# Optimization experiments

Hardware: AMD Instinct MI355X
Metric: run time of the kernel (lower is better)

## Reference

```python
import jax, jax.numpy as jnp
import numpy as np

EMBED_DIM = 1024
NUM_HEADS = 16
HEAD_DIM = EMBED_DIM // NUM_HEADS


def setup_inputs() -> dict:
    key = jax.random.key(0)
    ks = jax.random.split(key, 5)
    x = jax.random.normal(ks[0], (2, 2048, EMBED_DIM), dtype=jnp.float32)
    s_in = 1.0 / np.sqrt(EMBED_DIM)
    W_qkv = jax.random.uniform(ks[1], (EMBED_DIM, 3 * EMBED_DIM), minval=-s_in, maxval=s_in, dtype=jnp.float32)
    b_qkv = jax.random.uniform(ks[2], (3 * EMBED_DIM,), minval=-s_in, maxval=s_in, dtype=jnp.float32)
    W_out = jax.random.uniform(ks[3], (EMBED_DIM, EMBED_DIM), minval=-s_in, maxval=s_in, dtype=jnp.float32)
    b_out = jax.random.uniform(ks[4], (EMBED_DIM,), minval=-s_in, maxval=s_in, dtype=jnp.float32)
    return {"x": x, "W_qkv": W_qkv, "b_qkv": b_qkv, "W_out": W_out, "b_out": b_out}


def reference(x, W_qkv, b_qkv, W_out, b_out):
    B, S, D = x.shape
    H, Dh = NUM_HEADS, HEAD_DIM
    qkv = x @ W_qkv + b_qkv                       # [B, S, 3D]
    q, k, v = jnp.split(qkv, 3, axis=-1)
    # [B, S, D] -> [B, H, S, Dh]
    q = q.reshape(B, S, H, Dh).transpose(0, 2, 1, 3)
    k = k.reshape(B, S, H, Dh).transpose(0, 2, 1, 3)
    v = v.reshape(B, S, H, Dh).transpose(0, 2, 1, 3)
    scores = jnp.einsum('bhqd,bhkd->bhqk', q, k) / jnp.sqrt(jnp.float32(Dh))
    probs = jax.nn.softmax(scores, axis=-1)       # [B, H, S, S]
    attn = jnp.einsum('bhqk,bhkd->bhqd', probs, v)
    attn = attn.transpose(0, 2, 1, 3).reshape(B, S, D)
    return attn @ W_out + b_out
```

## Files before the change

kernel.cpp:

```cpp
#include <hip/hip_runtime.h>
#include <hip/hip_bf16.h>

#define DEV __device__ __forceinline__

typedef __bf16 bf16x8 __attribute__((ext_vector_type(8)));
typedef float f32x4 __attribute__((ext_vector_type(4)));
typedef float f32x16 __attribute__((ext_vector_type(16)));
using u16 = unsigned short;
using u32 = unsigned int;

static constexpr int S = 2048;
static constexpr int D = 1024;
static constexpr float SCQ = 0.125f * 1.44269504088896340736f;

DEV u16 f2bf(float f) {
  unsigned u = __builtin_bit_cast(unsigned, f);
  u += 0x7fffu + ((u >> 16) & 1u);
  return (u16)(u >> 16);
}
DEV u16 f2bfr(float f) {
  return (u16)((__builtin_bit_cast(u32, f) + 0x8000u) >> 16);
}
DEV u32 pk2(float a, float b) {
  u32 ua = __builtin_bit_cast(u32, a) + 0x8000u;
  u32 ub = __builtin_bit_cast(u32, b) + 0x8000u;
  return __builtin_amdgcn_perm(ub, ua, 0x07060302);
}

__global__ __launch_bounds__(256) void k_prep(const float* __restrict__ x, u16* __restrict__ Xb,
                                              const float* __restrict__ Wqkv, u16* __restrict__ WqkvT,
                                              const float* __restrict__ Wout, u16* __restrict__ WoutT) {
  __shared__ float t[32][33];
  const int bid = blockIdx.x;
  const int tid = threadIdx.x;
  if (bid < 4096) {
    const int i = bid * 256 + tid;
    const float4 v = reinterpret_cast<const float4*>(x)[i];
    ushort4 o;
    o.x = f2bf(v.x); o.y = f2bf(v.y); o.z = f2bf(v.z); o.w = f2bf(v.w);
    reinterpret_cast<ushort4*>(Xb)[i] = o;
    return;
  }
  const float* in;
  u16* out;
  int R, C, bx, by;
  if (bid < 4096 + 3072) {
    const int b = bid - 4096;
    in = Wqkv; out = WqkvT; R = 1024; C = 3072;
    bx = b % 96; by = b / 96;
  } else {
    const int b = bid - 7168;
    in = Wout; out = WoutT; R = 1024; C = 1024;
    bx = b & 31; by = b >> 5;
  }
  const int tx = tid & 31, ty = tid >> 5;
  const int c0 = bx * 32, r0 = by * 32;
  for (int i = ty; i < 32; i += 8)
    t[i][tx] = in[(size_t)(r0 + i) * C + c0 + tx];
  __syncthreads();
  for (int i = ty; i < 32; i += 8)
    out[(size_t)(c0 + i) * R + r0 + tx] = f2bf(t[tx][i]);
}

template <int MODE, int TN>
__global__ __launch_bounds__(256) void k_gemm(const u16* __restrict__ A, const u16* __restrict__ Bt,
                                              const float* __restrict__ bias, int M, int N, int K,
                                              u16* __restrict__ Qb, u16* __restrict__ Kb,
                                              u16* __restrict__ Vt, float* __restrict__ outF) {
  constexpr int NJ = TN / 32;
  __shared__ u16 As[128][40];
  __shared__ u16 Bs[TN][40];
  const int tid = threadIdx.x;
  const int lane = tid & 63, wave = tid >> 6;
  const int l15 = lane & 15, quad = lane >> 4;
  const int m0 = blockIdx.y * 128, n0 = blockIdx.x * TN;
  const int wm = (wave >> 1) * 64, wn = (wave & 1) * (TN / 2);
  const int row0 = tid >> 2, c0 = (tid & 3) * 8;
  const int row1 = row0 + 64;

  f32x4 acc[4][NJ];
#pragma unroll
  for (int i = 0; i < 4; i++)
#pragma unroll
    for (int j = 0; j < NJ; j++) acc[i][j] = (f32x4){0.f, 0.f, 0.f, 0.f};

  uint4 pa0 = *reinterpret_cast<const uint4*>(&A[(size_t)(m0 + row0) * K + c0]);
  uint4 pa1 = *reinterpret_cast<const uint4*>(&A[(size_t)(m0 + row1) * K + c0]);
  uint4 pb0 = *reinterpret_cast<const uint4*>(&Bt[(size_t)(n0 + row0) * K + c0]);
  uint4 pb1;
  if constexpr (TN == 128) pb1 = *reinterpret_cast<const uint4*>(&Bt[(size_t)(n0 + row1) * K + c0]);

  for (int kk = 0; kk < K; kk += 32) {
    __syncthreads();
    *reinterpret_cast<uint4*>(&As[row0][c0]) = pa0;
    *reinterpret_cast<uint4*>(&As[row1][c0]) = pa1;
    *reinterpret_cast<uint4*>(&Bs[row0 & (TN - 1)][c0]) = pb0;
    if constexpr (TN == 128) *reinterpret_cast<uint4*>(&Bs[row1][c0]) = pb1;
    __syncthreads();
    if (kk + 32 < K) {
      pa0 = *reinterpret_cast<const uint4*>(&A[(size_t)(m0 + row0) * K + kk + 32 + c0]);
      pa1 = *reinterpret_cast<const uint4*>(&A[(size_t)(m0 + row1) * K + kk + 32 + c0]);
      pb0 = *reinterpret_cast<const uint4*>(&Bt[(size_t)(n0 + row0) * K + kk + 32 + c0]);
      if constexpr (TN == 128)
        pb1 = *reinterpret_cast<const uint4*>(&Bt[(size_t)(n0 + row1) * K + kk + 32 + c0]);
    }
    bf16x8 af[4], bfv[NJ];
#pragma unroll
    for (int i = 0; i < 4; i++)
      af[i] = *reinterpret_cast<const bf16x8*>(&As[wm + i * 16 + l15][quad * 8]);
#pragma unroll
    for (int j = 0; j < NJ; j++)
      bfv[j] = *reinterpret_cast<const bf16x8*>(&Bs[wn + j * 16 + l15][quad * 8]);
#pragma unroll
    for (int i = 0; i < 4; i++)
#pragma unroll
      for (int j = 0; j < NJ; j++)
        acc[i][j] = __builtin_amdgcn_mfma_f32_16x16x32_bf16(af[i], bfv[j], acc[i][j], 0, 0, 0);
  }

  if constexpr (MODE == 0) {
    __shared__ u16 LT[64][136];
    if (n0 >= 2048) {
      const int b = m0 >> 11, sbase = m0 & 2047;
#pragma unroll
      for (int p = 0; p < 2; p++) {
        __syncthreads();
        if ((wave & 1) == p) {
#pragma unroll
          for (int j = 0; j < NJ; j++) {
            const int n = n0 + wn + j * 16 + l15;
            const float vb = bias[n];
#pragma unroll
            for (int i = 0; i < 4; i++) {
              uint2 pw;
              pw.x = pk2(acc[i][j][0] + vb, acc[i][j][1] + vb);
              pw.y = pk2(acc[i][j][2] + vb, acc[i][j][3] + vb);
              *reinterpret_cast<uint2*>(&LT[j * 16 + l15][wm + i * 16 + quad * 4]) = pw;
            }
          }
        }
        __syncthreads();
        const int h = ((n0 - 2048) >> 6) + p;
        const int bh = b * 16 + h;
        const int nl = tid >> 2, cc = (tid & 3) * 32;
        u16* dst = &Vt[((size_t)bh * 64 + nl) * S + sbase + cc];
#pragma unroll
        for (int k = 0; k < 4; k++)
          reinterpret_cast<uint4*>(dst)[k] = *reinterpret_cast<const uint4*>(&LT[nl][cc + k * 8]);
      }
    } else {
#pragma unroll
      for (int i = 0; i < 4; i++) {
#pragma unroll
        for (int j = 0; j < NJ; j++) {
#pragma unroll
          for (int r = 0; r < 4; r++) {
            const int m = m0 + wm + i * 16 + quad * 4 + r;
            const int n = n0 + wn + j * 16 + l15;
            const float v = acc[i][j][r] + bias[n];
            const int h = (n >> 6) & 15, dh = n & 63;
            const int b = m >> 11, s = m & 2047;
            const int bh = b * 16 + h;
            if (n < 1024) Qb[((size_t)bh * S + s) * 64 + dh] = f2bfr(v * SCQ);
            else          Kb[((size_t)bh * S + s) * 64 + dh] = f2bfr(v);
          }
        }
      }
    }
  } else {
#pragma unroll
    for (int i = 0; i < 4; i++)
#pragma unroll
      for (int j = 0; j < NJ; j++)
#pragma unroll
        for (int r = 0; r < 4; r++) {
          const int m = m0 + wm + i * 16 + quad * 4 + r;
          const int n = n0 + wn + j * 16 + l15;
          outF[(size_t)m * N + n] = acc[i][j][r] + bias[n];
        }
  }
}

__global__ __launch_bounds__(256, 2) void k_attn(const u16* __restrict__ Qb,
                                                 const u16* __restrict__ Kb,
                                                 const u16* __restrict__ Vt,
                                                 u16* __restrict__ attnB) {
  __shared__ u16 Ks[64][72];
  __shared__ u16 Vs[64][72];
  __shared__ u16 Pl[4][32][72];
  const int bh = blockIdx.y;
  const int q0 = blockIdx.x * 128;
  const int tid = threadIdx.x;
  const int lane = tid & 63, wave = tid >> 6;
  const int l31 = lane & 31, hi = lane >> 5;
  const u16* Qh = Qb + (size_t)bh * S * 64;
  const u16* Kh = Kb + (size_t)bh * S * 64;
  const u16* Vh = Vt + (size_t)bh * 64 * S;
  const int qrow = q0 + wave * 32 + l31;
  bf16x8 qf[4];
#pragma unroll
  for (int f = 0; f < 4; f++)
    qf[f] = *reinterpret_cast<const bf16x8*>(&Qh[(size_t)qrow * 64 + f * 16 + hi * 8]);

  const int r0 = tid >> 3, c0 = (tid & 7) * 8;

  float li = 0.f;
  f32x16 o0, o1;
#pragma unroll
  for (int r = 0; r < 16; r++) { o0[r] = 0.f; o1[r] = 0.f; }

  uint4 pk0 = *reinterpret_cast<const uint4*>(&Kh[(size_t)r0 * 64 + c0]);
  uint4 pk1 = *reinterpret_cast<const uint4*>(&Kh[(size_t)(r0 + 32) * 64 + c0]);
  uint4 pv0 = *reinterpret_cast<const uint4*>(&Vh[(size_t)r0 * S + c0]);
  uint4 pv1 = *reinterpret_cast<const uint4*>(&Vh[(size_t)(r0 + 32) * S + c0]);

  for (int kb = 0; kb < S / 64; kb++) {
    __syncthreads();
    *reinterpret_cast<uint4*>(&Ks[r0][c0]) = pk0;
    *reinterpret_cast<uint4*>(&Ks[r0 + 32][c0]) = pk1;
    *reinterpret_cast<uint4*>(&Vs[r0][c0]) = pv0;
    *reinterpret_cast<uint4*>(&Vs[r0 + 32][c0]) = pv1;
    __syncthreads();
    if (kb + 1 < S / 64) {
      const u16* Kn = Kh + (size_t)(kb + 1) * 64 * 64;
      pk0 = *reinterpret_cast<const uint4*>(&Kn[(size_t)r0 * 64 + c0]);
      pk1 = *reinterpret_cast<const uint4*>(&Kn[(size_t)(r0 + 32) * 64 + c0]);
      pv0 = *reinterpret_cast<const uint4*>(&Vh[(size_t)r0 * S + (kb + 1) * 64 + c0]);
      pv1 = *reinterpret_cast<const uint4*>(&Vh[(size_t)(r0 + 32) * S + (kb + 1) * 64 + c0]);
    }
    f32x16 z[2];
#pragma unroll
    for (int kt = 0; kt < 2; kt++) {
#pragma unroll
      for (int r = 0; r < 16; r++) z[kt][r] = 0.f;
#pragma unroll
      for (int f = 0; f < 4; f++) {
        const bf16x8 a = *reinterpret_cast<const bf16x8*>(&Ks[kt * 32 + l31][f * 16 + hi * 8]);
        z[kt] = __builtin_amdgcn_mfma_f32_32x32x16_bf16(a, qf[f], z[kt], 0, 0, 0);
      }
    }
    float s0 = 0.f, s1 = 0.f, s2 = 0.f, s3 = 0.f;
#pragma unroll
    for (int kt = 0; kt < 2; kt++)
#pragma unroll
      for (int r = 0; r < 16; r++) {
        const float p = __builtin_amdgcn_exp2f(z[kt][r]);
        z[kt][r] = p;
        if ((r & 3) == 0) s0 += p; else if ((r & 3) == 1) s1 += p;
        else if ((r & 3) == 2) s2 += p; else s3 += p;
      }
    li += (s0 + s1) + (s2 + s3);
#pragma unroll
    for (int kt = 0; kt < 2; kt++)
#pragma unroll
      for (int g = 0; g < 4; g++) {
        uint2 pw;
        pw.x = pk2(z[kt][g * 4 + 0], z[kt][g * 4 + 1]);
        pw.y = pk2(z[kt][g * 4 + 2], z[kt][g * 4 + 3]);
        *reinterpret_cast<uint2*>(&Pl[wave][l31][kt * 32 + g * 8 + hi * 4]) = pw;
      }
#pragma unroll
    for (int f = 0; f < 4; f++) {
      const bf16x8 bp = *reinterpret_cast<const bf16x8*>(&Pl[wave][l31][f * 16 + hi * 8]);
      const bf16x8 av0 = *reinterpret_cast<const bf16x8*>(&Vs[l31][f * 16 + hi * 8]);
      const bf16x8 av1 = *reinterpret_cast<const bf16x8*>(&Vs[32 + l31][f * 16 + hi * 8]);
      o0 = __builtin_amdgcn_mfma_f32_32x32x16_bf16(av0, bp, o0, 0, 0, 0);
      o1 = __builtin_amdgcn_mfma_f32_32x32x16_bf16(av1, bp, o1, 0, 0, 0);
    }
  }
  li += __shfl_xor(li, 32);
  const float inv = 1.f / li;
#pragma unroll
  for (int dt = 0; dt < 2; dt++) {
    const f32x16& od = dt ? o1 : o0;
#pragma unroll
    for (int g = 0; g < 4; g++) {
      uint2 ow;
      ow.x = pk2(od[g * 4 + 0] * inv, od[g * 4 + 1] * inv);
      ow.y = pk2(od[g * 4 + 2] * inv, od[g * 4 + 3] * inv);
      *reinterpret_cast<uint2*>(&Pl[wave][l31][dt * 32 + g * 8 + hi * 4]) = ow;
    }
  }
  const int b = bh >> 4, h = bh & 15;
  const int mbase = b * S + q0 + wave * 32;
  const int qr = lane >> 1, ch = (lane & 1) * 32;
  u16* dst = &attnB[(size_t)(mbase + qr) * D + h * 64 + ch];
#pragma unroll
  for (int c = 0; c < 4; c++)
    reinterpret_cast<uint4*>(dst)[c] = *reinterpret_cast<const uint4*>(&Pl[wave][qr][ch + c * 8]);
}

extern "C" void kernel_launch(void* const* d_in, const int* in_sizes, int n_in,
                              void* d_out, int out_size, void* d_ws, size_t ws_size,
                              hipStream_t stream) {
  const float* x = (const float*)d_in[0];
  const float* Wqkv = (const float*)d_in[1];
  const float* bqkv = (const float*)d_in[2];
  const float* Wout = (const float*)d_in[3];
  const float* bout = (const float*)d_in[4];
  float* out = (float*)d_out;

  char* p = (char*)d_ws;
  u16* Xb = (u16*)p;    p += (size_t)4096 * 1024 * 2;
  u16* WqkvT = (u16*)p; p += (size_t)3072 * 1024 * 2;
  u16* WoutT = (u16*)p; p += (size_t)1024 * 1024 * 2;
  u16* Qb = (u16*)p;    p += (size_t)32 * 2048 * 64 * 2;
  u16* Kb = (u16*)p;    p += (size_t)32 * 2048 * 64 * 2;
  u16* Vt = (u16*)p;    p += (size_t)32 * 64 * 2048 * 2;
  u16* attnB = (u16*)p; p += (size_t)4096 * 1024 * 2;

  k_prep<<<4096 + 3072 + 1024, 256, 0, stream>>>(x, Xb, Wqkv, WqkvT, Wout, WoutT);
  k_gemm<0, 128><<<dim3(3072 / 128, 4096 / 128), 256, 0, stream>>>(
      Xb, WqkvT, bqkv, 4096, 3072, 1024, Qb, Kb, Vt, nullptr);
  k_attn<<<dim3(2048 / 128, 32), 256, 0, stream>>>(Qb, Kb, Vt, attnB);
  k_gemm<1, 64><<<dim3(1024 / 64, 4096 / 128), 256, 0, stream>>>(
      attnB, WoutT, bout, 4096, 1024, 1024, nullptr, nullptr, nullptr, out);
}
```

Measured before the change: 199.9 us.

## Load GEMM tiles directly into LDS with global_load_lds

Replaces the register-staged global-to-LDS copy in the projection GEMM with direct global_load_lds transfers. The LDS rows lose their padding (stride 32 instead of 40), and a second barrier after the MFMAs guards buffer reuse. This removes the VGPR round trip and the LDS store instructions. In exchange it drops the register prefetch overlap, since each iteration now waits for the load before computing, and the unpadded layout may add bank conflicts on fragment reads.

```diff
diff --git a/kernel.cpp b/kernel.cpp
--- a/kernel.cpp
+++ b/kernel.cpp
@@ -25,6 +25,11 @@
   u32 ua = __builtin_bit_cast(u32, a) + 0x8000u;
   u32 ub = __builtin_bit_cast(u32, b) + 0x8000u;
   return __builtin_amdgcn_perm(ub, ua, 0x07060302);
+}
+
+DEV void gl16(const u16* __restrict__ g, u16* l) {
+  __builtin_amdgcn_global_load_lds((const __attribute__((address_space(1))) u32*)g,
+                                   (__attribute__((address_space(3))) u32*)l, 16, 0, 0);
 }
 
 __global__ __launch_bounds__(256) void k_prep(const float* __restrict__ x, u16* __restrict__ Xb,
@@ -68,15 +73,15 @@
                                               u16* __restrict__ Qb, u16* __restrict__ Kb,
                                               u16* __restrict__ Vt, float* __restrict__ outF) {
   constexpr int NJ = TN / 32;
-  __shared__ u16 As[128][40];
-  __shared__ u16 Bs[TN][40];
+  __shared__ u16 As[128][32];
+  __shared__ u16 Bs[TN][32];
   const int tid = threadIdx.x;
   const int lane = tid & 63, wave = tid >> 6;
   const int l15 = lane & 15, quad = lane >> 4;
   const int m0 = blockIdx.y * 128, n0 = blockIdx.x * TN;
   const int wm = (wave >> 1) * 64, wn = (wave & 1) * (TN / 2);
-  const int row0 = tid >> 2, c0 = (tid & 3) * 8;
-  const int row1 = row0 + 64;
+  const int lr = lane >> 2;
+  const int lc = (lane & 3) * 8;
 
   f32x4 acc[4][NJ];
 #pragma unroll
@@ -84,26 +89,27 @@
 #pragma unroll
     for (int j = 0; j < NJ; j++) acc[i][j] = (f32x4){0.f, 0.f, 0.f, 0.f};
 
-  uint4 pa0 = *reinterpret_cast<const uint4*>(&A[(size_t)(m0 + row0) * K + c0]);
-  uint4 pa1 = *reinterpret_cast<const uint4*>(&A[(size_t)(m0 + row1) * K + c0]);
-  uint4 pb0 = *reinterpret_cast<const uint4*>(&Bt[(size_t)(n0 + row0) * K + c0]);
-  uint4 pb1;
-  if constexpr (TN == 128) pb1 = *reinterpret_cast<const uint4*>(&Bt[(size_t)(n0 + row1) * K + c0]);
+  const u16* Aw0 = &A[(size_t)(m0 + wave * 32 + lr) * K + lc];
+  const u16* Aw1 = &A[(size_t)(m0 + wave * 32 + 16 + lr) * K + lc];
+  const u16* Bw0;
+  const u16* Bw1;
+  if constexpr (TN == 128) {
+    Bw0 = &Bt[(size_t)(n0 + wave * 32 + lr) * K + lc];
+    Bw1 = &Bt[(size_t)(n0 + wave * 32 + 16 + lr) * K + lc];
+  } else {
+    Bw0 = &Bt[(size_t)(n0 + wave * 16 + lr) * K + lc];
+  }
 
   for (int kk = 0; kk < K; kk += 32) {
+    gl16(Aw0 + kk, &As[wave * 32][0]);
+    gl16(Aw1 + kk, &As[wave * 32 + 16][0]);
+    if constexpr (TN == 128) {
+      gl16(Bw0 + kk, &Bs[wave * 32][0]);
+      gl16(Bw1 + kk, &Bs[wave * 32 + 16][0]);
+    } else {
+      gl16(Bw0 + kk, &Bs[wave * 16][0]);
+    }
     __syncthreads();
-    *reinterpret_cast<uint4*>(&As[row0][c0]) = pa0;
-    *reinterpret_cast<uint4*>(&As[row1][c0]) = pa1;
-    *reinterpret_cast<uint4*>(&Bs[row0 & (TN - 1)][c0]) = pb0;
-    if constexpr (TN == 128) *reinterpret_cast<uint4*>(&Bs[row1][c0]) = pb1;
-    __syncthreads();
-    if (kk + 32 < K) {
-      pa0 = *reinterpret_cast<const uint4*>(&A[(size_t)(m0 + row0) * K + kk + 32 + c0]);
-      pa1 = *reinterpret_cast<const uint4*>(&A[(size_t)(m0 + row1) * K + kk + 32 + c0]);
-      pb0 = *reinterpret_cast<const uint4*>(&Bt[(size_t)(n0 + row0) * K + kk + 32 + c0]);
-      if constexpr (TN == 128)
-        pb1 = *reinterpret_cast<const uint4*>(&Bt[(size_t)(n0 + row1) * K + kk + 32 + c0]);
-    }
     bf16x8 af[4], bfv[NJ];
 #pragma unroll
     for (int i = 0; i < 4; i++)
@@ -116,6 +122,7 @@
 #pragma unroll
       for (int j = 0; j < NJ; j++)
         acc[i][j] = __builtin_amdgcn_mfma_f32_16x16x32_bf16(af[i], bfv[j], acc[i][j], 0, 0, 0);
+    __syncthreads();
   }
 
   if constexpr (MODE == 0) {
```

New measurement: 209.5 us. +4.8%, slower.
